# Kernel tuning notes

Measured on AMD Instinct MI355X. Metric: run time of the kernel, lower is better.

## Reference

```python
import jax, jax.numpy as jnp
import numpy as np

B, T, E, H, V = 64, 32, 512, 512, 32000


def setup_inputs() -> dict:
    key = jax.random.key(0)
    ks = jax.random.split(key, 9)
    s = 0.05
    return {
        "features": jax.random.normal(ks[0], (B, E), jnp.float32),
        "captions": jax.random.randint(ks[1], (B, T), 0, V),
        "seq_len": T,
        "embed_table": jax.random.normal(ks[2], (V, E), jnp.float32) * s,
        "W_ih": jax.random.normal(ks[3], (4 * H, E), jnp.float32) * s,
        "W_hh": jax.random.normal(ks[4], (4 * H, H), jnp.float32) * s,
        "b_ih": jax.random.normal(ks[5], (4 * H,), jnp.float32) * s,
        "b_hh": jax.random.normal(ks[6], (4 * H,), jnp.float32) * s,
        "W_out": jax.random.normal(ks[7], (V, H), jnp.float32) * s,
        "b_out": jax.random.normal(ks[8], (V,), jnp.float32) * s,
    }


def _lstm_cell(x, h, c, W_ih, W_hh, b_ih, b_hh):
    # gates: (B, 4H), PyTorch LSTMCell gate order i, f, g, o
    gates = x @ W_ih.T + b_ih + h @ W_hh.T + b_hh
    i, f, g, o = jnp.split(gates, 4, axis=-1)
    c_new = jax.nn.sigmoid(f) * c + jax.nn.sigmoid(i) * jnp.tanh(g)
    h_new = jax.nn.sigmoid(o) * jnp.tanh(c_new)
    return h_new, c_new


def reference(features, captions, seq_len, embed_table, W_ih, W_hh, b_ih, b_hh, W_out, b_out):
    batch = features.shape[0]
    hdim = W_hh.shape[1]
    h0 = jnp.zeros((batch, hdim), features.dtype)
    c0 = jnp.zeros((batch, hdim), features.dtype)
    # prime the state with image features
    h, c = _lstm_cell(features, h0, c0, W_ih, W_hh, b_ih, b_hh)

    cap_emb = embed_table[captions]          # (B, T, E)
    xs = jnp.swapaxes(cap_emb, 0, 1)         # (T, B, E) for scan

    def step(carry, x_t):
        h, c = carry
        h, c = _lstm_cell(x_t, h, c, W_ih, W_hh, b_ih, b_hh)
        # dropout is identity in eval mode
        out = h @ W_out.T + b_out             # (B, V)
        return (h, c), out

    _, outs = jax.lax.scan(step, (h, c), xs)  # (T, B, V)
    return jnp.swapaxes(outs, 0, 1)           # (B, T, V)
```

## Files before the change

### kernel.cpp

```cpp
#include <hip/hip_runtime.h>
#include <stdint.h>

#define BB 64
#define TT 32
#define EE 512
#define HH 512
#define VV 32000
#define G4 2048

typedef _Float16 f16x8 __attribute__((ext_vector_type(8)));
typedef float f32x4 __attribute__((ext_vector_type(4)));

__device__ __forceinline__ unsigned short f2h(float f) {
  return __builtin_bit_cast(unsigned short, (_Float16)f);
}
__device__ __forceinline__ void gload_lds16(const unsigned short* g, unsigned short* l) {
  __builtin_amdgcn_global_load_lds((const __attribute__((address_space(1))) void*)g,
                                   (__attribute__((address_space(3))) void*)l, 16, 0, 0);
}
__device__ __forceinline__ float sigm(float x) { return 1.f / (1.f + __expf(-x)); }
__device__ __forceinline__ float tanh_fast(float x) {
  return 1.f - 2.f / (__expf(2.f * x) + 1.f);
}

__global__ __launch_bounds__(256) void k_gemm_ih(const float* __restrict__ feat,
                                                 const int* __restrict__ cap,
                                                 const float* __restrict__ emb,
                                                 const float* __restrict__ Bw,
                                                 const float* __restrict__ bih,
                                                 const float* __restrict__ bhh,
                                                 float* __restrict__ C) {
  __shared__ float As[16][128];
  __shared__ float Bs[16][128];
  const int tid = threadIdx.x;
  const int bx = blockIdx.x & 15;
  const int by = blockIdx.x >> 4;
  const int m0 = by * 128, n0 = bx * 128;
  const int tx = tid & 15, ty = tid >> 4;

  float acc[8][8];
#pragma unroll
  for (int i = 0; i < 8; i++)
#pragma unroll
    for (int j = 0; j < 8; j++) acc[i][j] = 0.f;

  const int lr = tid >> 1;
  const int lk = (tid & 1) * 8;
  int arow = m0 + lr; if (arow > 2111) arow = 2111;
  const float* Ap;
  if (arow < BB) {
    Ap = feat + (size_t)arow * EE + lk;
  } else {
    int idx = arow - BB;
    int t = idx >> 6, b = idx & 63;
    Ap = emb + (size_t)cap[b * TT + t] * EE + lk;
  }
  const int brow = n0 + lr;
  const float* Bp = Bw + (size_t)brow * EE + lk;

  for (int k0 = 0; k0 < EE; k0 += 16) {
    float4 a0 = *(const float4*)(Ap + k0);
    float4 a1 = *(const float4*)(Ap + k0 + 4);
    float4 b0 = *(const float4*)(Bp + k0);
    float4 b1 = *(const float4*)(Bp + k0 + 4);
    __syncthreads();
    As[lk + 0][lr] = a0.x; As[lk + 1][lr] = a0.y; As[lk + 2][lr] = a0.z; As[lk + 3][lr] = a0.w;
    As[lk + 4][lr] = a1.x; As[lk + 5][lr] = a1.y; As[lk + 6][lr] = a1.z; As[lk + 7][lr] = a1.w;
    Bs[lk + 0][lr] = b0.x; Bs[lk + 1][lr] = b0.y; Bs[lk + 2][lr] = b0.z; Bs[lk + 3][lr] = b0.w;
    Bs[lk + 4][lr] = b1.x; Bs[lk + 5][lr] = b1.y; Bs[lk + 6][lr] = b1.z; Bs[lk + 7][lr] = b1.w;
    __syncthreads();
#pragma unroll
    for (int k = 0; k < 16; k++) {
      float a[8], b[8];
      *(float4*)&a[0] = *(const float4*)&As[k][ty * 8];
      *(float4*)&a[4] = *(const float4*)&As[k][ty * 8 + 4];
      *(float4*)&b[0] = *(const float4*)&Bs[k][tx * 8];
      *(float4*)&b[4] = *(const float4*)&Bs[k][tx * 8 + 4];
#pragma unroll
      for (int i = 0; i < 8; i++)
#pragma unroll
        for (int j = 0; j < 8; j++) acc[i][j] += a[i] * b[j];
    }
  }

  float bs[8];
#pragma unroll
  for (int j = 0; j < 8; j++) {
    int n = n0 + tx * 8 + j;
    bs[j] = bih[n] + bhh[n];
  }
#pragma unroll
  for (int i = 0; i < 8; i++) {
    int m = m0 + ty * 8 + i;
    if (m < 2112) {
      float4 o0, o1;
      o0.x = acc[i][0] + bs[0]; o0.y = acc[i][1] + bs[1];
      o0.z = acc[i][2] + bs[2]; o0.w = acc[i][3] + bs[3];
      o1.x = acc[i][4] + bs[4]; o1.y = acc[i][5] + bs[5];
      o1.z = acc[i][6] + bs[6]; o1.w = acc[i][7] + bs[7];
      *(float4*)(C + (size_t)m * G4 + n0 + tx * 8) = o0;
      *(float4*)(C + (size_t)m * G4 + n0 + tx * 8 + 4) = o1;
    }
  }
}

__global__ void k_zero(int* f) {
  for (int i = threadIdx.x; i < 2560; i += 256)
    __hip_atomic_store(&f[i], 0, __ATOMIC_RELAXED, __HIP_MEMORY_SCOPE_AGENT);
}

__device__ __forceinline__ void agg_phase(int* arr, int* done, int tid, int p) {
  if (tid < 64) {
    for (;;) {
      int v = __hip_atomic_load(&arr[tid * 32], __ATOMIC_RELAXED, __HIP_MEMORY_SCOPE_AGENT);
      if (__all(v >= p)) break;
      __builtin_amdgcn_s_sleep(1);
    }
    if (tid == 0) {
#pragma unroll
      for (int c = 0; c < 16; ++c)
        __hip_atomic_store(&done[c * 32], p, __ATOMIC_RELAXED, __HIP_MEMORY_SCOPE_AGENT);
    }
  }
}

__device__ __forceinline__ void tree_wait(int* arr, int* done, int bid, int tid, int p) {
  if (bid == 0) {
    agg_phase(arr, done, tid, p);
  } else if (tid == 0) {
    while (__hip_atomic_load(&done[(bid & 15) * 32], __ATOMIC_RELAXED,
                             __HIP_MEMORY_SCOPE_AGENT) < p)
      __builtin_amdgcn_s_sleep(1);
  }
  __syncthreads();
}

__global__ __launch_bounds__(512) void k_fused(const float* __restrict__ Gpre,
                                               const float* __restrict__ Whh,
                                               const float* __restrict__ Wout,
                                               const float* __restrict__ bout,
                                               char* hseq_base,
                                               float* __restrict__ out,
                                               int* __restrict__ flags) {
  __shared__ __align__(16) char lds_raw[65536];
  unsigned short* hseq16 = (unsigned short*)hseq_base;
  unsigned int* hseq32 = (unsigned int*)hseq_base;
  int* arr = flags;
  int* done = flags + 2048;

  const int tid = threadIdx.x;
  const int bid = blockIdx.x;
  const int l = tid & 63;
  const int w = tid >> 6;

  if (bid < 64) {
    unsigned short* W_lds = (unsigned short*)lds_raw;
    float* gate_buf = (float*)(lds_raw + 32768);
    const int u0 = bid * 8;
    const int lr = l & 15;
    const int kc = l >> 4;
    const int nt = w & 1;
    const int mt = w >> 1;
    const int es = w * 8 + (l >> 3);
    const int edu = l & 7;

    {
      int row = tid >> 4;
      int sub = tid & 15;
      int g = row >> 3, du = row & 7;
      const float* srcp = Whh + (size_t)(g * 512 + u0 + du) * HH;
#pragma unroll
      for (int c0 = 0; c0 < 4; ++c0) {
        int c = sub * 4 + c0;
        float4 va = *(const float4*)(srcp + c * 8);
        float4 vb = *(const float4*)(srcp + c * 8 + 4);
        __align__(16) unsigned short t8[8];
        t8[0] = f2h(va.x); t8[1] = f2h(va.y); t8[2] = f2h(va.z); t8[3] = f2h(va.w);
        t8[4] = f2h(vb.x); t8[5] = f2h(vb.y); t8[6] = f2h(vb.z); t8[7] = f2h(vb.w);
        *(int4*)((char*)W_lds + row * 1024 + ((c ^ (row & 7)) * 16)) = *(const int4*)t8;
      }
    }

    float c_reg;
    {
      const float* gp = Gpre + (size_t)es * G4 + u0 + edu;
      float gi = gp[0], gg = gp[1024], go = gp[1536];
      float cn = sigm(gi) * tanh_fast(gg);
      float hn = sigm(go) * tanh_fast(cn);
      c_reg = cn;
      unsigned int hb = f2h(hn);
      unsigned int other = (unsigned int)__shfl_xor((int)hb, 1);
      if (!(l & 1))
        __hip_atomic_store(&hseq32[(size_t)es * 256 + bid * 4 + (edu >> 1)],
                           hb | (other << 16), __ATOMIC_RELAXED, __HIP_MEMORY_SCOPE_AGENT);
    }
    asm volatile("s_waitcnt vmcnt(0)" ::: "memory");
    __syncthreads();
    if (tid == 0)
      __hip_atomic_store(&arr[bid * 32], 1, __ATOMIC_RELAXED, __HIP_MEMORY_SCOPE_AGENT);

    float pre[4];
#pragma unroll
    for (int g = 0; g < 4; ++g)
      pre[g] = Gpre[((size_t)64 + es) * G4 + g * 512 + u0 + edu];

    tree_wait(arr, done, bid, tid, 1);

    for (int s = 1; s <= TT; ++s) {
      const unsigned short* hin = hseq16 + (size_t)(s - 1) * BB * HH;
      f32x4 acca = {0.f, 0.f, 0.f, 0.f};
      f32x4 accb = {0.f, 0.f, 0.f, 0.f};
      const unsigned short* hbase = hin + (size_t)(mt * 16 + lr) * HH + kc * 8;
      const int wrow = nt * 16 + lr;
      const char* wbase = (const char*)W_lds + wrow * 1024;
#pragma unroll
      for (int kk = 0; kk < 8; ++kk) {
        uint4 hq0 = *(const uint4*)(hbase + kk * 32);
        int4 wq0 = *(const int4*)(wbase + (((kk * 4 + kc) ^ (wrow & 7)) * 16));
        acca = __builtin_amdgcn_mfma_f32_16x16x32_f16(
            __builtin_bit_cast(f16x8, hq0), __builtin_bit_cast(f16x8, wq0), acca, 0, 0, 0);
        uint4 hq1 = *(const uint4*)(hbase + (kk + 8) * 32);
        int4 wq1 = *(const int4*)(wbase + ((((kk + 8) * 4 + kc) ^ (wrow & 7)) * 16));
        accb = __builtin_amdgcn_mfma_f32_16x16x32_f16(
            __builtin_bit_cast(f16x8, hq1), __builtin_bit_cast(f16x8, wq1), accb, 0, 0, 0);
      }
      f32x4 acc;
#pragma unroll
      for (int j = 0; j < 4; ++j) acc[j] = acca[j] + accb[j];

      {
        int g = nt * 2 + (lr >> 3);
        int du = lr & 7;
#pragma unroll
        for (int j = 0; j < 4; ++j) {
          int ss = mt * 16 + kc * 4 + j;
          gate_buf[g * 512 + du * 64 + (ss ^ (du << 3))] = acc[j];
        }
      }
      __syncthreads();

      {
        float gi = gate_buf[0 * 512 + edu * 64 + (es ^ (edu << 3))] + pre[0];
        float gf = gate_buf[1 * 512 + edu * 64 + (es ^ (edu << 3))] + pre[1];
        float gg = gate_buf[2 * 512 + edu * 64 + (es ^ (edu << 3))] + pre[2];
        float go = gate_buf[3 * 512 + edu * 64 + (es ^ (edu << 3))] + pre[3];
        float cn = sigm(gf) * c_reg + sigm(gi) * tanh_fast(gg);
        float hn = sigm(go) * tanh_fast(cn);
        c_reg = cn;
        unsigned int hb = f2h(hn);
        unsigned int other = (unsigned int)__shfl_xor((int)hb, 1);
        if (!(l & 1))
          __hip_atomic_store(&hseq32[(size_t)s * 16384 + es * 256 + bid * 4 + (edu >> 1)],
                             hb | (other << 16), __ATOMIC_RELAXED, __HIP_MEMORY_SCOPE_AGENT);
      }
      asm volatile("s_waitcnt vmcnt(0)" ::: "memory");
      __syncthreads();
      if (tid == 0)
        __hip_atomic_store(&arr[bid * 32], s + 1, __ATOMIC_RELAXED, __HIP_MEMORY_SCOPE_AGENT);

      if (s < TT) {
#pragma unroll
        for (int g = 0; g < 4; ++g)
          pre[g] = Gpre[((size_t)(s + 1) * 64 + es) * G4 + g * 512 + u0 + edu];
        tree_wait(arr, done, bid, tid, s + 1);
      }
    }

    if (bid == 0) agg_phase(arr, done, tid, TT + 1);
  } else {
    unsigned short* As = (unsigned short*)lds_raw;
    const int slice0 = bid - 64;
    const bool two = (slice0 < 58);
    const int n00 = slice0 * 128;
    const int n01 = (two ? (slice0 + 192) : slice0) * 128;
    const int bcol = w * 16 + (l >> 4) * 4;
    const float4 bo0 = *(const float4*)(bout + n00 + bcol);
    const float4 bo1 = *(const float4*)(bout + n01 + bcol);

    const int vr0 = n00 + w * 16 + (l & 15);
    const int vr1 = n01 + w * 16 + (l & 15);
    const int kb = (l >> 4) * 8;
    uint4 w0r[16], w1r[16];
#pragma unroll
    for (int kt = 0; kt < 16; ++kt) {
      const float* p = Wout + (size_t)vr0 * HH + kt * 32 + kb;
      float4 a = *(const float4*)p;
      float4 b = *(const float4*)(p + 4);
      __align__(16) unsigned short t8[8];
      t8[0] = f2h(a.x); t8[1] = f2h(a.y); t8[2] = f2h(a.z); t8[3] = f2h(a.w);
      t8[4] = f2h(b.x); t8[5] = f2h(b.y); t8[6] = f2h(b.z); t8[7] = f2h(b.w);
      w0r[kt] = *(const uint4*)t8;
    }
    if (two) {
#pragma unroll
      for (int kt = 0; kt < 16; ++kt) {
        const float* p = Wout + (size_t)vr1 * HH + kt * 32 + kb;
        float4 a = *(const float4*)p;
        float4 b = *(const float4*)(p + 4);
        __align__(16) unsigned short t8[8];
        t8[0] = f2h(a.x); t8[1] = f2h(a.y); t8[2] = f2h(a.z); t8[3] = f2h(a.w);
        t8[4] = f2h(b.x); t8[5] = f2h(b.y); t8[6] = f2h(b.z); t8[7] = f2h(b.w);
        w1r[kt] = *(const uint4*)t8;
      }
    }

    for (int s = 1; s <= TT; ++s) {
      if (tid == 0) {
        while (__hip_atomic_load(&done[(bid & 15) * 32], __ATOMIC_RELAXED,
                                 __HIP_MEMORY_SCOPE_AGENT) < s + 1)
          __builtin_amdgcn_s_sleep(2);
      }
      __syncthreads();

      const unsigned short* hs = hseq16 + (size_t)s * BB * HH;
#pragma unroll
      for (int it = 0; it < 8; ++it) {
        int ci = it * 512 + tid;
        int row = ci >> 6, cd = ci & 63;
        gload_lds16(hs + (size_t)row * 512 + (cd ^ (row & 7)) * 8, As + ci * 8);
      }
      asm volatile("s_waitcnt vmcnt(0)" ::: "memory");
      __syncthreads();

      f32x4 acc0[4], acc1[4];
#pragma unroll
      for (int m = 0; m < 4; ++m) {
        acc0[m] = (f32x4){0.f, 0.f, 0.f, 0.f};
        acc1[m] = (f32x4){0.f, 0.f, 0.f, 0.f};
      }
#pragma unroll
      for (int m = 0; m < 4; ++m) {
        int row = m * 16 + (l & 15);
#pragma unroll
        for (int kt = 0; kt < 16; ++kt) {
          int c = kt * 4 + (l >> 4);
          f16x8 af = *(const f16x8*)&As[row * 512 + (c ^ (row & 7)) * 8];
          acc0[m] = __builtin_amdgcn_mfma_f32_16x16x32_f16(
              __builtin_bit_cast(f16x8, w0r[kt]), af, acc0[m], 0, 0, 0);
          if (two)
            acc1[m] = __builtin_amdgcn_mfma_f32_16x16x32_f16(
                __builtin_bit_cast(f16x8, w1r[kt]), af, acc1[m], 0, 0, 0);
        }
      }

#pragma unroll
      for (int m = 0; m < 4; ++m) {
        int b = m * 16 + (l & 15);
        float* orow0 = out + ((size_t)(b * TT + (s - 1))) * VV + n00 + bcol;
        float4 v;
        v.x = acc0[m][0] + bo0.x;
        v.y = acc0[m][1] + bo0.y;
        v.z = acc0[m][2] + bo0.z;
        v.w = acc0[m][3] + bo0.w;
        *(float4*)orow0 = v;
        if (two) {
          float* orow1 = out + ((size_t)(b * TT + (s - 1))) * VV + n01 + bcol;
          float4 v1;
          v1.x = acc1[m][0] + bo1.x;
          v1.y = acc1[m][1] + bo1.y;
          v1.z = acc1[m][2] + bo1.z;
          v1.w = acc1[m][3] + bo1.w;
          *(float4*)orow1 = v1;
        }
      }
    }
  }
}

extern "C" void kernel_launch(void* const* d_in, const int* in_sizes, int n_in,
                              void* d_out, int out_size, void* d_ws, size_t ws_size,
                              hipStream_t stream) {
  const float* feat = (const float*)d_in[0];
  const int* cap = (const int*)d_in[1];
  const float* emb = (const float*)d_in[3];
  const float* Wih = (const float*)d_in[4];
  const float* Whh = (const float*)d_in[5];
  const float* bih = (const float*)d_in[6];
  const float* bhh = (const float*)d_in[7];
  const float* Wout = (const float*)d_in[8];
  const float* bout = (const float*)d_in[9];
  float* out = (float*)d_out;

  char* ws = (char*)d_ws;
  float* Gpre = (float*)ws;
  char* hseq = ws + 17301504;
  int* flags = (int*)(ws + 19464192);

  k_zero<<<dim3(1), dim3(256), 0, stream>>>(flags);
  k_gemm_ih<<<dim3(17 * 16), dim3(256), 0, stream>>>(feat, cap, emb, Wih, bih, bhh, Gpre);
  k_fused<<<dim3(256), dim3(512), 0, stream>>>(Gpre, Whh, Wout, bout, hseq, out, flags);
}
```

Measured before the change: 448.1 us.

## Relay hidden state through per-XCC copy with one elected relay block

Each output-projection block reads its XCC id, and one block per XCC is elected through a compare-exchange to act as relay. At each step the relay waits on the global done flag, copies the step's fp16 hidden state into a per-XCC buffer, and raises a per-XCC flag. The other blocks wait on that local flag and load from the relay copy. This is meant to cut cross-XCC polling and coherence traffic, at the cost of an extra copy and an added serial hop on the recurrence critical path.

```diff
diff --git a/kernel.cpp b/kernel.cpp
--- a/kernel.cpp
+++ b/kernel.cpp
@@ -105,7 +105,7 @@
 }
 
 __global__ void k_zero(int* f) {
-  for (int i = threadIdx.x; i < 2560; i += 256)
+  for (int i = threadIdx.x; i < 3072; i += 256)
     __hip_atomic_store(&f[i], 0, __ATOMIC_RELAXED, __HIP_MEMORY_SCOPE_AGENT);
 }
 
@@ -140,9 +140,11 @@
                                                const float* __restrict__ Wout,
                                                const float* __restrict__ bout,
                                                char* hseq_base,
+                                               unsigned short* __restrict__ hrelay,
                                                float* __restrict__ out,
                                                int* __restrict__ flags) {
   __shared__ __align__(16) char lds_raw[65536];
+  __shared__ int relay_sh;
   unsigned short* hseq16 = (unsigned short*)hseq_base;
   unsigned int* hseq32 = (unsigned int*)hseq_base;
   int* arr = flags;
@@ -277,6 +279,21 @@
     const float4 bo0 = *(const float4*)(bout + n00 + bcol);
     const float4 bo1 = *(const float4*)(bout + n01 + bcol);
 
+    int xcc;
+    asm volatile("s_getreg_b32 %0, hwreg(HW_REG_XCC_ID)" : "=s"(xcc));
+    xcc &= 7;
+    int* xflag = flags + 2560 + xcc * 32;
+    int* claim = flags + 2816 + xcc * 32;
+    if (tid == 0) {
+      int expected = 0;
+      bool won = __hip_atomic_compare_exchange_strong(
+          claim, &expected, 1, __ATOMIC_RELAXED, __ATOMIC_RELAXED, __HIP_MEMORY_SCOPE_AGENT);
+      relay_sh = won ? 1 : 0;
+    }
+    __syncthreads();
+    const bool isRelay = (relay_sh != 0);
+    unsigned short* hrbase = hrelay + (size_t)xcc * 33 * (BB * HH);
+
     const int vr0 = n00 + w * 16 + (l & 15);
     const int vr1 = n01 + w * 16 + (l & 15);
     const int kb = (l >> 4) * 8;
@@ -305,19 +322,42 @@
     }
 
     for (int s = 1; s <= TT; ++s) {
-      if (tid == 0) {
-        while (__hip_atomic_load(&done[(bid & 15) * 32], __ATOMIC_RELAXED,
-                                 __HIP_MEMORY_SCOPE_AGENT) < s + 1)
-          __builtin_amdgcn_s_sleep(2);
-      }
-      __syncthreads();
-
       const unsigned short* hs = hseq16 + (size_t)s * BB * HH;
-#pragma unroll
-      for (int it = 0; it < 8; ++it) {
-        int ci = it * 512 + tid;
-        int row = ci >> 6, cd = ci & 63;
-        gload_lds16(hs + (size_t)row * 512 + (cd ^ (row & 7)) * 8, As + ci * 8);
+      unsigned short* hr = hrbase + (size_t)s * (BB * HH);
+
+      if (isRelay) {
+        if (tid == 0) {
+          while (__hip_atomic_load(&done[(bid & 15) * 32], __ATOMIC_RELAXED,
+                                   __HIP_MEMORY_SCOPE_AGENT) < s + 1)
+            __builtin_amdgcn_s_sleep(2);
+        }
+        __syncthreads();
+#pragma unroll
+        for (int it = 0; it < 8; ++it)
+          ((uint4*)hr)[it * 512 + tid] = ((const uint4*)hs)[it * 512 + tid];
+        asm volatile("s_waitcnt vmcnt(0)" ::: "memory");
+        __syncthreads();
+        if (tid == 0)
+          __hip_atomic_store(xflag, s + 1, __ATOMIC_RELAXED, __HIP_MEMORY_SCOPE_AGENT);
+#pragma unroll
+        for (int it = 0; it < 8; ++it) {
+          int ci = it * 512 + tid;
+          int row = ci >> 6, cd = ci & 63;
+          gload_lds16(hs + (size_t)row * 512 + (cd ^ (row & 7)) * 8, As + ci * 8);
+        }
+      } else {
+        if (tid == 0) {
+          while (__hip_atomic_load(xflag, __ATOMIC_RELAXED,
+                                   __HIP_MEMORY_SCOPE_AGENT) < s + 1)
+            __builtin_amdgcn_s_sleep(2);
+        }
+        __syncthreads();
+#pragma unroll
+        for (int it = 0; it < 8; ++it) {
+          int ci = it * 512 + tid;
+          int row = ci >> 6, cd = ci & 63;
+          gload_lds16(hr + (size_t)row * 512 + (cd ^ (row & 7)) * 8, As + ci * 8);
+        }
       }
       asm volatile("s_waitcnt vmcnt(0)" ::: "memory");
       __syncthreads();
@@ -385,8 +425,9 @@
   float* Gpre = (float*)ws;
   char* hseq = ws + 17301504;
   int* flags = (int*)(ws + 19464192);
+  unsigned short* hrelay = (unsigned short*)(ws + 20971520);
 
   k_zero<<<dim3(1), dim3(256), 0, stream>>>(flags);
   k_gemm_ih<<<dim3(17 * 16), dim3(256), 0, stream>>>(feat, cap, emb, Wih, bih, bhh, Gpre);
-  k_fused<<<dim3(256), dim3(512), 0, stream>>>(Gpre, Whh, Wout, bout, hseq, out, flags);
-}
+  k_fused<<<dim3(256), dim3(512), 0, stream>>>(Gpre, Whh, Wout, bout, hseq, hrelay, out, flags);
+}
```

Result: slower. 482.8 us (+7.8%).

## Split fused kernel into XCC-local recurrent kernel and separate output GEMM

Applied to the files above, without the earlier changes.

Replaces the single fused kernel, where 64 blocks ran the LSTM recurrence while the remaining blocks overlapped the vocabulary projection, with two kernels. The recurrence now runs on 16 blocks that claim slots only if they sit on XCC 0, so the per-step barrier traffic stays within one chiplet's L2; each block handles 32 hidden units with gates exchanged through shuffles instead of LDS. The output projection then runs afterwards as a plain 250-block GEMM over all timesteps. This trades the overlap of projection with recurrence for cheaper cross-block synchronisation, and relies on enough blocks landing on XCC 0; otherwise the barrier deadlocks.

```diff
diff --git a/kernel.cpp b/kernel.cpp
--- a/kernel.cpp
+++ b/kernel.cpp
@@ -7,6 +7,7 @@
 #define HH 512
 #define VV 32000
 #define G4 2048
+#define NRNN 16
 
 typedef _Float16 f16x8 __attribute__((ext_vector_type(8)));
 typedef float f32x4 __attribute__((ext_vector_type(4)));
@@ -104,265 +105,234 @@
   }
 }
 
-__global__ void k_zero(int* f) {
-  for (int i = threadIdx.x; i < 2560; i += 256)
-    __hip_atomic_store(&f[i], 0, __ATOMIC_RELAXED, __HIP_MEMORY_SCOPE_AGENT);
-}
-
-__device__ __forceinline__ void agg_phase(int* arr, int* done, int tid, int p) {
-  if (tid < 64) {
-    for (;;) {
-      int v = __hip_atomic_load(&arr[tid * 32], __ATOMIC_RELAXED, __HIP_MEMORY_SCOPE_AGENT);
-      if (__all(v >= p)) break;
-      __builtin_amdgcn_s_sleep(1);
-    }
-    if (tid == 0) {
-#pragma unroll
-      for (int c = 0; c < 16; ++c)
-        __hip_atomic_store(&done[c * 32], p, __ATOMIC_RELAXED, __HIP_MEMORY_SCOPE_AGENT);
-    }
-  }
-}
-
-__device__ __forceinline__ void tree_wait(int* arr, int* done, int bid, int tid, int p) {
-  if (bid == 0) {
-    agg_phase(arr, done, tid, p);
+__device__ __forceinline__ void bar_wait(int* arr, int* done, int slot, int tid, int p) {
+  if (slot == 0) {
+    if (tid < 64) {
+      for (;;) {
+        int v = (tid < NRNN)
+                    ? __hip_atomic_load(&arr[tid * 32], __ATOMIC_RELAXED, __HIP_MEMORY_SCOPE_AGENT)
+                    : p;
+        if (__all(v >= p)) break;
+        __builtin_amdgcn_s_sleep(1);
+      }
+      if (tid < 4)
+        __hip_atomic_store(&done[tid * 32], p, __ATOMIC_RELAXED, __HIP_MEMORY_SCOPE_AGENT);
+    }
   } else if (tid == 0) {
-    while (__hip_atomic_load(&done[(bid & 15) * 32], __ATOMIC_RELAXED,
+    while (__hip_atomic_load(&done[(slot & 3) * 32], __ATOMIC_RELAXED,
                              __HIP_MEMORY_SCOPE_AGENT) < p)
       __builtin_amdgcn_s_sleep(1);
   }
   __syncthreads();
 }
 
-__global__ __launch_bounds__(512) void k_fused(const float* __restrict__ Gpre,
-                                               const float* __restrict__ Whh,
-                                               const float* __restrict__ Wout,
-                                               const float* __restrict__ bout,
-                                               char* hseq_base,
-                                               float* __restrict__ out,
-                                               int* __restrict__ flags) {
-  __shared__ __align__(16) char lds_raw[65536];
-  unsigned short* hseq16 = (unsigned short*)hseq_base;
-  unsigned int* hseq32 = (unsigned int*)hseq_base;
-  int* arr = flags;
-  int* done = flags + 2048;
-
+__global__ __launch_bounds__(512) void k_rnn(const float* __restrict__ Gpre,
+                                             const float* __restrict__ Whh,
+                                             unsigned short* __restrict__ hseq,
+                                             int* __restrict__ flags) {
+  __shared__ __align__(16) unsigned short W_lds[128 * 512];
+  __shared__ int slot_sh;
   const int tid = threadIdx.x;
-  const int bid = blockIdx.x;
+
+  if (tid == 0) {
+    int xcc;
+    asm volatile("s_getreg_b32 %0, hwreg(HW_REG_XCC_ID)" : "=s"(xcc));
+    int slot = -1;
+    if ((xcc & 7) == 0)
+      slot = __hip_atomic_fetch_add(&flags[512], 1, __ATOMIC_RELAXED, __HIP_MEMORY_SCOPE_AGENT);
+    slot_sh = slot;
+  }
+  __syncthreads();
+  const int slot = slot_sh;
+  if (slot < 0 || slot >= NRNN) return;
+
   const int l = tid & 63;
   const int w = tid >> 6;
-
-  if (bid < 64) {
-    unsigned short* W_lds = (unsigned short*)lds_raw;
-    float* gate_buf = (float*)(lds_raw + 32768);
-    const int u0 = bid * 8;
-    const int lr = l & 15;
-    const int kc = l >> 4;
-    const int nt = w & 1;
-    const int mt = w >> 1;
-    const int es = w * 8 + (l >> 3);
-    const int edu = l & 7;
-
-    {
-      int row = tid >> 4;
-      int sub = tid & 15;
-      int g = row >> 3, du = row & 7;
-      const float* srcp = Whh + (size_t)(g * 512 + u0 + du) * HH;
-#pragma unroll
-      for (int c0 = 0; c0 < 4; ++c0) {
-        int c = sub * 4 + c0;
-        float4 va = *(const float4*)(srcp + c * 8);
-        float4 vb = *(const float4*)(srcp + c * 8 + 4);
-        __align__(16) unsigned short t8[8];
-        t8[0] = f2h(va.x); t8[1] = f2h(va.y); t8[2] = f2h(va.z); t8[3] = f2h(va.w);
-        t8[4] = f2h(vb.x); t8[5] = f2h(vb.y); t8[6] = f2h(vb.z); t8[7] = f2h(vb.w);
-        *(int4*)((char*)W_lds + row * 1024 + ((c ^ (row & 7)) * 16)) = *(const int4*)t8;
-      }
-    }
-
-    float c_reg;
-    {
-      const float* gp = Gpre + (size_t)es * G4 + u0 + edu;
-      float gi = gp[0], gg = gp[1024], go = gp[1536];
-      float cn = sigm(gi) * tanh_fast(gg);
-      float hn = sigm(go) * tanh_fast(cn);
-      c_reg = cn;
-      unsigned int hb = f2h(hn);
-      unsigned int other = (unsigned int)__shfl_xor((int)hb, 1);
-      if (!(l & 1))
-        __hip_atomic_store(&hseq32[(size_t)es * 256 + bid * 4 + (edu >> 1)],
-                           hb | (other << 16), __ATOMIC_RELAXED, __HIP_MEMORY_SCOPE_AGENT);
-    }
+  const int lr = l & 15;
+  const int kc = l >> 4;
+  const int d = l & 3;
+  const int u0 = slot * 32;
+  const int u = u0 + w * 4 + d;
+  int* arr = flags;
+  int* done = flags + 1024;
+
+#pragma unroll
+  for (int it = 0; it < 16; ++it) {
+    int id = it * 512 + tid;
+    int r = id >> 6, c = id & 63;
+    int wv = r >> 4, g = (r >> 2) & 3, du = r & 3;
+    const float* src = Whh + (size_t)(g * 512 + u0 + wv * 4 + du) * HH + c * 8;
+    float4 a = *(const float4*)src;
+    float4 b = *(const float4*)(src + 4);
+    __align__(16) unsigned short t8[8];
+    t8[0] = f2h(a.x); t8[1] = f2h(a.y); t8[2] = f2h(a.z); t8[3] = f2h(a.w);
+    t8[4] = f2h(b.x); t8[5] = f2h(b.y); t8[6] = f2h(b.z); t8[7] = f2h(b.w);
+    *(int4*)&W_lds[r * 512 + ((c ^ (r & 7)) * 8)] = *(const int4*)t8;
+  }
+
+  float c_reg[16];
+  if (lr < 4) {
+#pragma unroll
+    for (int mt = 0; mt < 4; ++mt)
+#pragma unroll
+      for (int j = 0; j < 4; ++j) {
+        int sample = mt * 16 + kc * 4 + j;
+        const float* gp = Gpre + (size_t)sample * G4;
+        float gi = gp[u], gg = gp[1024 + u], go = gp[1536 + u];
+        float cn = sigm(gi) * tanh_fast(gg);
+        float hn = sigm(go) * tanh_fast(cn);
+        c_reg[mt * 4 + j] = cn;
+        hseq[(size_t)sample * HH + u] = f2h(hn);
+      }
+  }
+  asm volatile("s_waitcnt vmcnt(0)" ::: "memory");
+  __syncthreads();
+  if (tid == 0)
+    __hip_atomic_store(&arr[slot * 32], 1, __ATOMIC_RELAXED, __HIP_MEMORY_SCOPE_AGENT);
+
+  float gpre[4][16];
+  if (lr < 4) {
+#pragma unroll
+    for (int mt = 0; mt < 4; ++mt)
+#pragma unroll
+      for (int j = 0; j < 4; ++j) {
+        int sample = mt * 16 + kc * 4 + j;
+        const float* gp = Gpre + (size_t)(1 * 64 + sample) * G4;
+        gpre[0][mt * 4 + j] = gp[u];
+        gpre[1][mt * 4 + j] = gp[512 + u];
+        gpre[2][mt * 4 + j] = gp[1024 + u];
+        gpre[3][mt * 4 + j] = gp[1536 + u];
+      }
+  }
+  bar_wait(arr, done, slot, tid, 1);
+
+  for (int s = 1; s <= TT; ++s) {
+    const unsigned short* hin = hseq + (size_t)(s - 1) * (BB * HH);
+    unsigned short* hout = hseq + (size_t)s * (BB * HH);
+
+    f32x4 acc[4];
+#pragma unroll
+    for (int mt = 0; mt < 4; ++mt) acc[mt] = (f32x4){0.f, 0.f, 0.f, 0.f};
+    const int wrow = w * 16 + lr;
+#pragma unroll
+    for (int kk = 0; kk < 16; ++kk) {
+      int4 wq = *(const int4*)&W_lds[wrow * 512 + (((kk * 4 + kc) ^ (lr & 7)) * 8)];
+      f16x8 wf = __builtin_bit_cast(f16x8, wq);
+#pragma unroll
+      for (int mt = 0; mt < 4; ++mt) {
+        uint4 hq = *(const uint4*)(hin + (size_t)(mt * 16 + lr) * HH + kk * 32 + kc * 8);
+        acc[mt] = __builtin_amdgcn_mfma_f32_16x16x32_f16(
+            __builtin_bit_cast(f16x8, hq), wf, acc[mt], 0, 0, 0);
+      }
+    }
+
+#pragma unroll
+    for (int mt = 0; mt < 4; ++mt)
+#pragma unroll
+      for (int j = 0; j < 4; ++j) {
+        float v = acc[mt][j];
+        float gi = __shfl(v, (kc << 4) + d);
+        float gf = __shfl(v, (kc << 4) + 4 + d);
+        float gg = __shfl(v, (kc << 4) + 8 + d);
+        float go = __shfl(v, (kc << 4) + 12 + d);
+        if (lr < 4) {
+          int sample = mt * 16 + kc * 4 + j;
+          gi += gpre[0][mt * 4 + j];
+          gf += gpre[1][mt * 4 + j];
+          gg += gpre[2][mt * 4 + j];
+          go += gpre[3][mt * 4 + j];
+          float cn = sigm(gf) * c_reg[mt * 4 + j] + sigm(gi) * tanh_fast(gg);
+          float hn = sigm(go) * tanh_fast(cn);
+          c_reg[mt * 4 + j] = cn;
+          hout[(size_t)sample * HH + u] = f2h(hn);
+        }
+      }
     asm volatile("s_waitcnt vmcnt(0)" ::: "memory");
     __syncthreads();
     if (tid == 0)
-      __hip_atomic_store(&arr[bid * 32], 1, __ATOMIC_RELAXED, __HIP_MEMORY_SCOPE_AGENT);
-
-    float pre[4];
-#pragma unroll
-    for (int g = 0; g < 4; ++g)
-      pre[g] = Gpre[((size_t)64 + es) * G4 + g * 512 + u0 + edu];
-
-    tree_wait(arr, done, bid, tid, 1);
-
-    for (int s = 1; s <= TT; ++s) {
-      const unsigned short* hin = hseq16 + (size_t)(s - 1) * BB * HH;
-      f32x4 acca = {0.f, 0.f, 0.f, 0.f};
-      f32x4 accb = {0.f, 0.f, 0.f, 0.f};
-      const unsigned short* hbase = hin + (size_t)(mt * 16 + lr) * HH + kc * 8;
-      const int wrow = nt * 16 + lr;
-      const char* wbase = (const char*)W_lds + wrow * 1024;
-#pragma unroll
-      for (int kk = 0; kk < 8; ++kk) {
-        uint4 hq0 = *(const uint4*)(hbase + kk * 32);
-        int4 wq0 = *(const int4*)(wbase + (((kk * 4 + kc) ^ (wrow & 7)) * 16));
-        acca = __builtin_amdgcn_mfma_f32_16x16x32_f16(
-            __builtin_bit_cast(f16x8, hq0), __builtin_bit_cast(f16x8, wq0), acca, 0, 0, 0);
-        uint4 hq1 = *(const uint4*)(hbase + (kk + 8) * 32);
-        int4 wq1 = *(const int4*)(wbase + ((((kk + 8) * 4 + kc) ^ (wrow & 7)) * 16));
-        accb = __builtin_amdgcn_mfma_f32_16x16x32_f16(
-            __builtin_bit_cast(f16x8, hq1), __builtin_bit_cast(f16x8, wq1), accb, 0, 0, 0);
-      }
-      f32x4 acc;
-#pragma unroll
-      for (int j = 0; j < 4; ++j) acc[j] = acca[j] + accb[j];
-
-      {
-        int g = nt * 2 + (lr >> 3);
-        int du = lr & 7;
-#pragma unroll
-        for (int j = 0; j < 4; ++j) {
-          int ss = mt * 16 + kc * 4 + j;
-          gate_buf[g * 512 + du * 64 + (ss ^ (du << 3))] = acc[j];
-        }
-      }
-      __syncthreads();
-
-      {
-        float gi = gate_buf[0 * 512 + edu * 64 + (es ^ (edu << 3))] + pre[0];
-        float gf = gate_buf[1 * 512 + edu * 64 + (es ^ (edu << 3))] + pre[1];
-        float gg = gate_buf[2 * 512 + edu * 64 + (es ^ (edu << 3))] + pre[2];
-        float go = gate_buf[3 * 512 + edu * 64 + (es ^ (edu << 3))] + pre[3];
-        float cn = sigm(gf) * c_reg + sigm(gi) * tanh_fast(gg);
-        float hn = sigm(go) * tanh_fast(cn);
-        c_reg = cn;
-        unsigned int hb = f2h(hn);
-        unsigned int other = (unsigned int)__shfl_xor((int)hb, 1);
-        if (!(l & 1))
-          __hip_atomic_store(&hseq32[(size_t)s * 16384 + es * 256 + bid * 4 + (edu >> 1)],
-                             hb | (other << 16), __ATOMIC_RELAXED, __HIP_MEMORY_SCOPE_AGENT);
-      }
-      asm volatile("s_waitcnt vmcnt(0)" ::: "memory");
-      __syncthreads();
-      if (tid == 0)
-        __hip_atomic_store(&arr[bid * 32], s + 1, __ATOMIC_RELAXED, __HIP_MEMORY_SCOPE_AGENT);
-
-      if (s < TT) {
-#pragma unroll
-        for (int g = 0; g < 4; ++g)
-          pre[g] = Gpre[((size_t)(s + 1) * 64 + es) * G4 + g * 512 + u0 + edu];
-        tree_wait(arr, done, bid, tid, s + 1);
-      }
-    }
-
-    if (bid == 0) agg_phase(arr, done, tid, TT + 1);
-  } else {
-    unsigned short* As = (unsigned short*)lds_raw;
-    const int slice0 = bid - 64;
-    const bool two = (slice0 < 58);
-    const int n00 = slice0 * 128;
-    const int n01 = (two ? (slice0 + 192) : slice0) * 128;
-    const int bcol = w * 16 + (l >> 4) * 4;
-    const float4 bo0 = *(const float4*)(bout + n00 + bcol);
-    const float4 bo1 = *(const float4*)(bout + n01 + bcol);
-
-    const int vr0 = n00 + w * 16 + (l & 15);
-    const int vr1 = n01 + w * 16 + (l & 15);
-    const int kb = (l >> 4) * 8;
-    uint4 w0r[16], w1r[16];
-#pragma unroll
-    for (int kt = 0; kt < 16; ++kt) {
-      const float* p = Wout + (size_t)vr0 * HH + kt * 32 + kb;
-      float4 a = *(const float4*)p;
-      float4 b = *(const float4*)(p + 4);
-      __align__(16) unsigned short t8[8];
-      t8[0] = f2h(a.x); t8[1] = f2h(a.y); t8[2] = f2h(a.z); t8[3] = f2h(a.w);
-      t8[4] = f2h(b.x); t8[5] = f2h(b.y); t8[6] = f2h(b.z); t8[7] = f2h(b.w);
-      w0r[kt] = *(const uint4*)t8;
-    }
-    if (two) {
+      __hip_atomic_store(&arr[slot * 32], s + 1, __ATOMIC_RELAXED, __HIP_MEMORY_SCOPE_AGENT);
+
+    if (s < TT) {
+      if (lr < 4) {
+#pragma unroll
+        for (int mt = 0; mt < 4; ++mt)
+#pragma unroll
+          for (int j = 0; j < 4; ++j) {
+            int sample = mt * 16 + kc * 4 + j;
+            const float* gp = Gpre + (size_t)((s + 1) * 64 + sample) * G4;
+            gpre[0][mt * 4 + j] = gp[u];
+            gpre[1][mt * 4 + j] = gp[512 + u];
+            gpre[2][mt * 4 + j] = gp[1024 + u];
+            gpre[3][mt * 4 + j] = gp[1536 + u];
+          }
+      }
+      bar_wait(arr, done, slot, tid, s + 1);
+    }
+  }
+}
+
+__global__ __launch_bounds__(512) void k_gemm_out(const unsigned short* __restrict__ hseq,
+                                                  const float* __restrict__ Wout,
+                                                  const float* __restrict__ bout,
+                                                  float* __restrict__ out) {
+  __shared__ __align__(16) unsigned short As[BB * HH];
+  const int tid = threadIdx.x;
+  const int l = tid & 63;
+  const int w = tid >> 6;
+  const int n00 = blockIdx.x * 128;
+  const int bcol = w * 16 + (l >> 4) * 4;
+  const float4 bo0 = *(const float4*)(bout + n00 + bcol);
+
+  const int vr0 = n00 + w * 16 + (l & 15);
+  const int kb = (l >> 4) * 8;
+  uint4 w0r[16];
+#pragma unroll
+  for (int kt = 0; kt < 16; ++kt) {
+    const float* p = Wout + (size_t)vr0 * HH + kt * 32 + kb;
+    float4 a = *(const float4*)p;
+    float4 b = *(const float4*)(p + 4);
+    __align__(16) unsigned short t8[8];
+    t8[0] = f2h(a.x); t8[1] = f2h(a.y); t8[2] = f2h(a.z); t8[3] = f2h(a.w);
+    t8[4] = f2h(b.x); t8[5] = f2h(b.y); t8[6] = f2h(b.z); t8[7] = f2h(b.w);
+    w0r[kt] = *(const uint4*)t8;
+  }
+
+  for (int s = 1; s <= TT; ++s) {
+    if (s > 1) __syncthreads();
+    const unsigned short* hs = hseq + (size_t)s * (BB * HH);
+#pragma unroll
+    for (int it = 0; it < 8; ++it) {
+      int ci = it * 512 + tid;
+      int row = ci >> 6, cd = ci & 63;
+      gload_lds16(hs + (size_t)row * HH + (cd ^ (row & 7)) * 8, As + ci * 8);
+    }
+    asm volatile("s_waitcnt vmcnt(0)" ::: "memory");
+    __syncthreads();
+
+    f32x4 acc0[4];
+#pragma unroll
+    for (int m = 0; m < 4; ++m) acc0[m] = (f32x4){0.f, 0.f, 0.f, 0.f};
+#pragma unroll
+    for (int m = 0; m < 4; ++m) {
+      int row = m * 16 + (l & 15);
 #pragma unroll
       for (int kt = 0; kt < 16; ++kt) {
-        const float* p = Wout + (size_t)vr1 * HH + kt * 32 + kb;
-        float4 a = *(const float4*)p;
-        float4 b = *(const float4*)(p + 4);
-        __align__(16) unsigned short t8[8];
-        t8[0] = f2h(a.x); t8[1] = f2h(a.y); t8[2] = f2h(a.z); t8[3] = f2h(a.w);
-        t8[4] = f2h(b.x); t8[5] = f2h(b.y); t8[6] = f2h(b.z); t8[7] = f2h(b.w);
-        w1r[kt] = *(const uint4*)t8;
-      }
-    }
-
-    for (int s = 1; s <= TT; ++s) {
-      if (tid == 0) {
-        while (__hip_atomic_load(&done[(bid & 15) * 32], __ATOMIC_RELAXED,
-                                 __HIP_MEMORY_SCOPE_AGENT) < s + 1)
-          __builtin_amdgcn_s_sleep(2);
-      }
-      __syncthreads();
-
-      const unsigned short* hs = hseq16 + (size_t)s * BB * HH;
-#pragma unroll
-      for (int it = 0; it < 8; ++it) {
-        int ci = it * 512 + tid;
-        int row = ci >> 6, cd = ci & 63;
-        gload_lds16(hs + (size_t)row * 512 + (cd ^ (row & 7)) * 8, As + ci * 8);
-      }
-      asm volatile("s_waitcnt vmcnt(0)" ::: "memory");
-      __syncthreads();
-
-      f32x4 acc0[4], acc1[4];
-#pragma unroll
-      for (int m = 0; m < 4; ++m) {
-        acc0[m] = (f32x4){0.f, 0.f, 0.f, 0.f};
-        acc1[m] = (f32x4){0.f, 0.f, 0.f, 0.f};
-      }
-#pragma unroll
-      for (int m = 0; m < 4; ++m) {
-        int row = m * 16 + (l & 15);
-#pragma unroll
-        for (int kt = 0; kt < 16; ++kt) {
-          int c = kt * 4 + (l >> 4);
-          f16x8 af = *(const f16x8*)&As[row * 512 + (c ^ (row & 7)) * 8];
-          acc0[m] = __builtin_amdgcn_mfma_f32_16x16x32_f16(
-              __builtin_bit_cast(f16x8, w0r[kt]), af, acc0[m], 0, 0, 0);
-          if (two)
-            acc1[m] = __builtin_amdgcn_mfma_f32_16x16x32_f16(
-                __builtin_bit_cast(f16x8, w1r[kt]), af, acc1[m], 0, 0, 0);
-        }
-      }
-
-#pragma unroll
-      for (int m = 0; m < 4; ++m) {
-        int b = m * 16 + (l & 15);
-        float* orow0 = out + ((size_t)(b * TT + (s - 1))) * VV + n00 + bcol;
-        float4 v;
-        v.x = acc0[m][0] + bo0.x;
-        v.y = acc0[m][1] + bo0.y;
-        v.z = acc0[m][2] + bo0.z;
-        v.w = acc0[m][3] + bo0.w;
-        *(float4*)orow0 = v;
-        if (two) {
-          float* orow1 = out + ((size_t)(b * TT + (s - 1))) * VV + n01 + bcol;
-          float4 v1;
-          v1.x = acc1[m][0] + bo1.x;
-          v1.y = acc1[m][1] + bo1.y;
-          v1.z = acc1[m][2] + bo1.z;
-          v1.w = acc1[m][3] + bo1.w;
-          *(float4*)orow1 = v1;
-        }
-      }
+        int c = kt * 4 + (l >> 4);
+        f16x8 af = *(const f16x8*)&As[row * HH + (c ^ (row & 7)) * 8];
+        acc0[m] = __builtin_amdgcn_mfma_f32_16x16x32_f16(
+            __builtin_bit_cast(f16x8, w0r[kt]), af, acc0[m], 0, 0, 0);
+      }
+    }
+#pragma unroll
+    for (int m = 0; m < 4; ++m) {
+      int b = m * 16 + (l & 15);
+      float* orow = out + ((size_t)(b * TT + (s - 1))) * VV + n00 + bcol;
+      float4 v;
+      v.x = acc0[m][0] + bo0.x;
+      v.y = acc0[m][1] + bo0.y;
+      v.z = acc0[m][2] + bo0.z;
+      v.w = acc0[m][3] + bo0.w;
+      *(float4*)orow = v;
     }
   }
 }
@@ -383,10 +353,11 @@
 
   char* ws = (char*)d_ws;
   float* Gpre = (float*)ws;
-  char* hseq = ws + 17301504;
+  unsigned short* hseq = (unsigned short*)(ws + 17301504);
   int* flags = (int*)(ws + 19464192);
 
-  k_zero<<<dim3(1), dim3(256), 0, stream>>>(flags);
+  hipMemsetAsync(flags, 0, 8192, stream);
   k_gemm_ih<<<dim3(17 * 16), dim3(256), 0, stream>>>(feat, cap, emb, Wih, bih, bhh, Gpre);
-  k_fused<<<dim3(256), dim3(512), 0, stream>>>(Gpre, Whh, Wout, bout, hseq, out, flags);
-}
+  k_rnn<<<dim3(256), dim3(512), 0, stream>>>(Gpre, Whh, hseq, flags);
+  k_gemm_out<<<dim3(250), dim3(512), 0, stream>>>(hseq, Wout, bout, out);
+}
```

After: 924.2 us. +106.3%, slower.
